# Performance work log

Hardware: AMD Instinct MI355X
Metric: run time of the kernel (lower is better)

## Reference

```python
import jax, jax.numpy as jnp
import numpy as np
from jax.scipy.linalg import solve_triangular

EPS = 2e-05  # module eps (original only adds it on Cholesky failure)
NUM_LABELS = 8


def setup_inputs() -> dict:
    key = jax.random.key(0)
    k1, k2, k3, k4 = jax.random.split(key, 4)
    B, N, H, W = 1, 256, 512, 512
    return {
        "content_feat": jax.random.normal(k1, (B, N, H, W), dtype=jnp.float32),
        "style_feat": jax.random.normal(k2, (B, N, H, W), dtype=jnp.float32),
        "content_seg": jax.random.randint(k3, (H, W), 0, NUM_LABELS, dtype=jnp.int32),
        "style_seg": jax.random.randint(k4, (H, W), 0, NUM_LABELS, dtype=jnp.int32),
        "num_labels": NUM_LABELS,
    }


def _cwct(c, s, seg_c, seg_s, num_labels):
    # c, s: (N, M) flattened features; seg_*: (M,) int labels
    N = c.shape[0]
    eye = jnp.eye(N, dtype=c.dtype)
    target = c
    for l in range(num_labels):  # fixed small label count
        mc = (seg_c == l)  # (Mc,) content mask
        ms = (seg_s == l)
        nc = mc.sum().astype(c.dtype)
        ns = ms.sum().astype(c.dtype)
        nc1 = jnp.maximum(nc, 1.0)
        ns1 = jnp.maximum(ns, 1.0)
        # masked mean + centered (zeros outside mask)
        mean_c = (c * mc).sum(-1) / nc1
        xc = (c - mean_c[:, None]) * mc  # (N, M)
        cov_c = (xc @ xc.T) / jnp.maximum(nc1 - 1.0, 1.0)  # (N, N)
        Lc = jnp.linalg.cholesky(cov_c)
        inv_Lc = solve_triangular(Lc, eye, lower=True)
        white = inv_Lc @ xc
        # style stats + coloring
        mean_s = (s * ms).sum(-1) / ns1
        xs = (s - mean_s[:, None]) * ms
        cov_s = (xs @ xs.T) / jnp.maximum(ns1 - 1.0, 1.0)
        Ls = jnp.linalg.cholesky(cov_s)
        colored = Ls @ white + mean_s[:, None]
        # label validity: >10 pixels each side, count ratio < 100
        valid = (nc > 10) & (ns > 10) & (nc < 100.0 * ns) & (ns < 100.0 * nc)
        target = jnp.where(mc[None, :] & valid, colored, target)
    return target


def reference(content_feat, style_feat, content_seg, style_seg, num_labels):
    B, N, cH, cW = content_feat.shape  # B == 1 (original code only supports B=1)
    c = content_feat.reshape(N, cH * cW)
    s = style_feat.reshape(N, -1)
    out = _cwct(c, s, content_seg.reshape(-1), style_seg.reshape(-1), num_labels)
    return out.reshape(B, N, cH, cW)
```

## Files before the change

### kernel.cpp

```cpp
#include <hip/hip_runtime.h>

#define NCH   256
#define M_PIX 262144
#define MPAD  266240
#define LDA   40

typedef short bf16x8 __attribute__((ext_vector_type(8)));
typedef float f32x4  __attribute__((ext_vector_type(4)));

__device__ __forceinline__ unsigned short f2bf(float f) {
  union { float f; unsigned u; } v; v.f = f;
  unsigned r = v.u + 0x7FFFu + ((v.u >> 16) & 1u);
  return (unsigned short)(r >> 16);
}
__device__ __forceinline__ float bf2f(unsigned short h) {
  union { unsigned u; float f; } v; v.u = ((unsigned)h) << 16;
  return v.f;
}

__global__ __launch_bounds__(256) void k_hist(const int* __restrict__ seg_c,
                                              const int* __restrict__ seg_s,
                                              int* __restrict__ hist) {
  __shared__ int h[16];
  int t = threadIdx.x;
  if (t < 16) h[t] = 0;
  __syncthreads();
  int p0 = blockIdx.x * 2048 + t * 8;
#pragma unroll
  for (int e = 0; e < 8; ++e) {
    atomicAdd(&h[seg_c[p0 + e] & 7], 1);
    atomicAdd(&h[8 + (seg_s[p0 + e] & 7)], 1);
  }
  __syncthreads();
  if (t < 8) hist[blockIdx.x * 8 + t] = h[t];
  else if (t < 16) hist[1024 + blockIdx.x * 8 + (t - 8)] = h[t];
}

__global__ __launch_bounds__(256) void k_scan(const int* __restrict__ hist,
                                              int* __restrict__ base,
                                              int* __restrict__ off,
                                              int* __restrict__ cnt,
                                              int* __restrict__ valid) {
  __shared__ int lh[2048];
  __shared__ int tot[16];
  __shared__ int loff[2][9];
  int t = threadIdx.x;
  for (int i = t; i < 2048; i += 256) lh[i] = hist[i];
  __syncthreads();
  if (t < 16) {
    int s = t >> 3, l = t & 7, acc = 0;
    for (int b = 0; b < 128; ++b) acc += lh[s * 1024 + b * 8 + l];
    tot[t] = acc;
  }
  __syncthreads();
  if (t < 2) {
    int run = 0;
    for (int l = 0; l < 8; ++l) {
      loff[t][l] = run;
      run = (run + tot[t * 8 + l] + 511) & ~511;
    }
    loff[t][8] = run;
    for (int l = 0; l < 9; ++l) off[t * 9 + l] = loff[t][l];
    for (int l = 0; l < 8; ++l) cnt[t * 8 + l] = tot[t * 8 + l];
  }
  __syncthreads();
  if (t < 8) {
    long nc = tot[t], ns = tot[8 + t];
    valid[t] = (nc > 10 && ns > 10 && nc < 100 * ns && ns < 100 * nc) ? 1 : 0;
  }
  if (t < 16) {
    int s = t >> 3, l = t & 7;
    int run = loff[s][l];
    for (int b = 0; b < 128; ++b) {
      base[s * 1024 + b * 8 + l] = run;
      run += lh[s * 1024 + b * 8 + l];
    }
  }
}

__global__ __launch_bounds__(256) void k_rank(const int* __restrict__ seg_c,
                                              const int* __restrict__ seg_s,
                                              const int* __restrict__ base,
                                              int* __restrict__ dst) {
  __shared__ int sc[8 * 272];
  __shared__ int rb[256 * 8];
  __shared__ int bb[8];
  int t = threadIdx.x;
  for (int s = 0; s < 2; ++s) {
    const int* seg = s ? seg_s : seg_c;
    const int* bas = base + s * 1024 + blockIdx.x * 8;
    int* dd = dst + (size_t)s * M_PIX;
    int p0 = blockIdx.x * 2048 + t * 8;
    unsigned pk2 = 0, cpk = 0;
#pragma unroll
    for (int e = 0; e < 8; ++e) {
      int lb = seg[p0 + e] & 7;
      pk2 |= (unsigned)lb << (3 * e);
      cpk += 1u << (4 * lb);
    }
#pragma unroll
    for (int lq = 0; lq < 8; ++lq) sc[lq * 272 + t] = (int)((cpk >> (4 * lq)) & 15u);
    if (t < 8) bb[t] = bas[t];
    __syncthreads();
    for (int d = 1; d < 256; d <<= 1) {
      int v[8];
#pragma unroll
      for (int lq = 0; lq < 8; ++lq)
        v[lq] = sc[lq * 272 + t] + ((t >= d) ? sc[lq * 272 + t - d] : 0);
      __syncthreads();
#pragma unroll
      for (int lq = 0; lq < 8; ++lq) sc[lq * 272 + t] = v[lq];
      __syncthreads();
    }
#pragma unroll
    for (int lq = 0; lq < 8; ++lq)
      rb[t * 8 + lq] = bb[lq] + sc[lq * 272 + t] - (int)((cpk >> (4 * lq)) & 15u);
#pragma unroll
    for (int e = 0; e < 8; ++e) {
      int lb = (int)((pk2 >> (3 * e)) & 7u);
      int dpos = rb[t * 8 + lb]++;
      dd[p0 + e] = dpos;
    }
    __syncthreads();
  }
}

__global__ __launch_bounds__(256) void k_padzero(unsigned short* __restrict__ P,
                                                 const int* __restrict__ off,
                                                 const int* __restrict__ cnt) {
  int l = blockIdx.x;
  int c0, c1;
  if (l < 8) { c0 = off[l] + cnt[l]; c1 = off[l + 1]; }
  else       { c0 = off[8];          c1 = MPAD; }
  int w = c1 - c0;
  if (w <= 0) return;
  for (int r = 0; r < 256; ++r)
    for (int cc = threadIdx.x; cc < w; cc += 256)
      P[(size_t)r * MPAD + c0 + cc] = 0;
}

__global__ __launch_bounds__(256) void k_pack(const float* __restrict__ feat,
                                              const int* __restrict__ seg,
                                              const int* __restrict__ dst,
                                              const int* __restrict__ base,
                                              unsigned short* __restrict__ P) {
  int b = blockIdx.x, g = blockIdx.y, t = threadIdx.x;
  int p0 = b * 2048;
  __shared__ unsigned short buf[8][2048];
  __shared__ int h[8], lbase[9], gbase[8];
  if (t < 8) { h[t] = 0; gbase[t] = base[b * 8 + t]; }
  __syncthreads();
  int lb[8], slot[8], gd[8];
#pragma unroll
  for (int i = 0; i < 8; ++i) {
    lb[i] = seg[p0 + i * 256 + t] & 7;
    atomicAdd(&h[lb[i]], 1);
  }
  __syncthreads();
  if (t == 0) {
    int run = 0;
    for (int l = 0; l < 8; ++l) { lbase[l] = run; run += h[l]; }
    lbase[8] = run;
  }
  __syncthreads();
#pragma unroll
  for (int i = 0; i < 8; ++i)
    slot[i] = lbase[lb[i]] + (dst[p0 + i * 256 + t] - gbase[lb[i]]);
#pragma unroll
  for (int i = 0; i < 8; ++i) {
    int q = i * 256 + t;
    int l = 0;
    while (l < 7 && q >= lbase[l + 1]) ++l;
    gd[i] = gbase[l] + q - lbase[l];
  }
  int n0 = g * 32;
#pragma unroll 1
  for (int cp = 0; cp < 4; ++cp) {
#pragma unroll
    for (int c = 0; c < 8; ++c) {
      const float* fp = &feat[(size_t)(n0 + cp * 8 + c) * M_PIX + p0];
#pragma unroll
      for (int i = 0; i < 8; ++i)
        buf[c][slot[i]] = f2bf(fp[i * 256 + t]);
    }
    __syncthreads();
#pragma unroll
    for (int c = 0; c < 8; ++c) {
      unsigned short* pp = &P[(size_t)(n0 + cp * 8 + c) * MPAD];
#pragma unroll
      for (int i = 0; i < 8; ++i)
        pp[gd[i]] = buf[c][i * 256 + t];
    }
    __syncthreads();
  }
}

__global__ __launch_bounds__(256) void k_unpack(const unsigned short* __restrict__ P,
                                                const int* __restrict__ seg,
                                                const int* __restrict__ dst,
                                                const int* __restrict__ base,
                                                float* __restrict__ out) {
  int b = blockIdx.x, g = blockIdx.y, t = threadIdx.x;
  int p0 = b * 2048;
  __shared__ unsigned short buf[8][2048];
  __shared__ int h[8], lbase[9], gbase[8];
  if (t < 8) { h[t] = 0; gbase[t] = base[b * 8 + t]; }
  __syncthreads();
  int lb[8], slot[8], gd[8];
#pragma unroll
  for (int i = 0; i < 8; ++i) {
    lb[i] = seg[p0 + i * 256 + t] & 7;
    atomicAdd(&h[lb[i]], 1);
  }
  __syncthreads();
  if (t == 0) {
    int run = 0;
    for (int l = 0; l < 8; ++l) { lbase[l] = run; run += h[l]; }
    lbase[8] = run;
  }
  __syncthreads();
#pragma unroll
  for (int i = 0; i < 8; ++i)
    slot[i] = lbase[lb[i]] + (dst[p0 + i * 256 + t] - gbase[lb[i]]);
#pragma unroll
  for (int i = 0; i < 8; ++i) {
    int q = i * 256 + t;
    int l = 0;
    while (l < 7 && q >= lbase[l + 1]) ++l;
    gd[i] = gbase[l] + q - lbase[l];
  }
  int n0 = g * 32;
#pragma unroll 1
  for (int cp = 0; cp < 4; ++cp) {
#pragma unroll
    for (int c = 0; c < 8; ++c) {
      const unsigned short* pp = &P[(size_t)(n0 + cp * 8 + c) * MPAD];
#pragma unroll
      for (int i = 0; i < 8; ++i)
        buf[c][i * 256 + t] = pp[gd[i]];
    }
    __syncthreads();
#pragma unroll
    for (int c = 0; c < 8; ++c) {
      float* op = &out[(size_t)(n0 + cp * 8 + c) * M_PIX + p0];
#pragma unroll
      for (int i = 0; i < 8; ++i)
        op[i * 256 + t] = bf2f(buf[c][slot[i]]);
    }
    __syncthreads();
  }
}

__global__ __launch_bounds__(512) void k_gram(const unsigned short* __restrict__ P,
                                              const int* __restrict__ off,
                                              float* __restrict__ G,
                                              float* __restrict__ sum) {
  int l = blockIdx.y;
  long o0 = off[l], o1 = off[l + 1];
  long k0 = o0 + (long)blockIdx.x * 1024;
  if (k0 >= o1) return;
  long rem = o1 - k0;
  int ks = rem > 1024 ? 1024 : (int)rem;

  __shared__ unsigned short Sb[256 * LDA];
  int t = threadIdx.x, wave = t >> 6, lane = t & 63;
  int wr = (wave < 2) ? wave * 64 : 128 + (wave & 1) * 64;
  int wc = (wave >= 4) ? 128 : 0;
  bool wact = (wave < 6);

  f32x4 acc[4][8] = {};
  float rsum = 0.0f;

  for (int kk = 0; kk < ks; kk += 32) {
#pragma unroll
    for (int it = 0; it < 2; ++it) {
      int slot = t + it * 512;
      int rr = slot >> 2, gg = slot & 3;
      *(uint4*)&Sb[rr * LDA + gg * 8] =
          *(const uint4*)&P[(size_t)rr * MPAD + (size_t)(k0 + kk) + gg * 8];
    }
    __syncthreads();
    if (t < 256) {
#pragma unroll
      for (int e = 0; e < 16; ++e) {
        unsigned v = *(const unsigned*)&Sb[t * LDA + e * 2];
        rsum += bf2f((unsigned short)(v & 0xFFFFu)) + bf2f((unsigned short)(v >> 16));
      }
    }
    if (wact) {
      bf16x8 bfr[8];
#pragma unroll
      for (int fj = 0; fj < 8; ++fj)
        bfr[fj] = *(const bf16x8*)&Sb[(wc + fj * 16 + (lane & 15)) * LDA + (lane >> 4) * 8];
#pragma unroll
      for (int fi = 0; fi < 4; ++fi) {
        bf16x8 afr = *(const bf16x8*)&Sb[(wr + fi * 16 + (lane & 15)) * LDA + (lane >> 4) * 8];
#pragma unroll
        for (int fj = 0; fj < 8; ++fj)
          acc[fi][fj] = __builtin_amdgcn_mfma_f32_16x16x32_bf16(afr, bfr[fj], acc[fi][fj], 0, 0, 0);
      }
    }
    __syncthreads();
  }
  float* Gl = G + ((size_t)l << 16);
  if (wact) {
#pragma unroll
    for (int fi = 0; fi < 4; ++fi)
#pragma unroll
      for (int fj = 0; fj < 8; ++fj) {
        int cc = wc + fj * 16 + (lane & 15);
#pragma unroll
        for (int rg = 0; rg < 4; ++rg) {
          int rr2 = wr + fi * 16 + (lane >> 4) * 4 + rg;
          atomicAdd(&Gl[rr2 * 256 + cc], acc[fi][fj][rg]);
        }
      }
  }
  if (t < 256) atomicAdd(&sum[l * 256 + t], rsum);
}

__global__ __launch_bounds__(256) void k_cov(float* __restrict__ G,
                                             const float* __restrict__ sum,
                                             const int* __restrict__ cnt,
                                             float* __restrict__ means) {
  int bid = blockIdx.x;
  float* A = G + ((size_t)bid << 16);
  int t = threadIdx.x;
  __shared__ float mu[256];
  float fc = (float)cnt[bid];
  float m = sum[bid * 256 + t] / fmaxf(fc, 1.0f);
  mu[t] = m;
  means[bid * 256 + t] = m;
  __syncthreads();
  float rdiv = 1.0f / fmaxf(fmaxf(fc, 1.0f) - 1.0f, 1.0f);
  float mt = mu[t];
  for (int i = t; i < 256; ++i) {
    float g = A[i * 256 + t];
    A[t * 256 + i] = (g - fc * mu[i] * mt) * rdiv;
  }
}

__global__ __launch_bounds__(256) void k_panel(float* __restrict__ G,
                                               float* __restrict__ Wg,
                                               int pb) {
  float* LT = G + ((size_t)blockIdx.x << 16);
  int t = threadIdx.x;
  int jbase = pb * 32;
  int H2 = 224 - jbase;
  __shared__ float Wl[32 * 36];

  if (t < 64) {
    int l32 = t & 31;
    float x[32];
#pragma unroll
    for (int k = 0; k < 32; ++k)
      x[k] = (k <= l32) ? LT[(size_t)(jbase + k) * 256 + jbase + l32] : 0.0f;
#pragma unroll
    for (int j = 0; j < 32; ++j) {
      float dj = __shfl(x[j], j, 64);
      float rd = 1.0f / sqrtf(dj);
      float lj = x[j] * rd;
      x[j] = lj;
#pragma unroll
      for (int k = j + 1; k < 32; ++k) {
        float lkj = __shfl(lj, k, 64);
        x[k] -= lj * lkj;
      }
    }
    if (t < 32) {
#pragma unroll
      for (int k = 0; k < 32; ++k)
        if (k <= l32) LT[(size_t)(jbase + k) * 256 + jbase + l32] = x[k];
    }
    float w[32];
#pragma unroll
    for (int k = 0; k < 32; ++k) w[k] = 0.0f;
#pragma unroll
    for (int i2 = 0; i2 < 32; ++i2) {
      float s = (i2 == l32) ? 1.0f : 0.0f;
#pragma unroll
      for (int k = 0; k < 32; ++k)
        if (k < i2) s -= __shfl(x[k], i2, 64) * w[k];
      float Lii = __shfl(x[i2], i2, 64);
      float wv = s / Lii;
      w[i2] = (i2 >= l32) ? wv : 0.0f;
    }
    if (t < 32) {
      float* Wgp = Wg + (((size_t)blockIdx.x * 8 + pb) << 10);
#pragma unroll
      for (int i2 = 0; i2 < 32; ++i2)
        if (i2 >= l32) {
          Wl[i2 * 36 + l32] = w[i2];
          Wgp[i2 * 32 + l32] = w[i2];
        }
    }
  }
  __syncthreads();

  if (t < H2) {
    int r = jbase + 32 + t;
    float a[32];
#pragma unroll
    for (int k = 0; k < 32; ++k) a[k] = LT[(size_t)(jbase + k) * 256 + r];
#pragma unroll
    for (int j = 0; j < 32; ++j) {
      float s = 0.0f;
#pragma unroll
      for (int k = 0; k < 32; ++k)
        if (k <= j) s += a[k] * Wl[j * 36 + k];
      LT[(size_t)(jbase + j) * 256 + r] = s;
    }
  }
}

__global__ __launch_bounds__(256) void k_trail(float* __restrict__ G, int pb) {
  int jbase = pb * 32;
  int H2 = 224 - jbase;
  int nts2 = (H2 + 63) >> 6;
  int y = blockIdx.y;
  if (y >= (nts2 * (nts2 + 1)) >> 1) return;
  int ti = 0;
  while ((((ti + 1) * (ti + 2)) >> 1) <= y) ++ti;
  int tj = y - ((ti * (ti + 1)) >> 1);
  float* LT = G + ((size_t)blockIdx.x << 16);
  int i0 = jbase + 32 + ti * 64;
  int j0 = jbase + 32 + tj * 64;

  __shared__ float Li[32][64];
  __shared__ float Lj[32][64];
  int t = threadIdx.x;
  for (int idx = t; idx < 2048; idx += 256) {
    int k = idx >> 6, r = idx & 63;
    Li[k][r] = (i0 + r < 256) ? LT[(size_t)(jbase + k) * 256 + i0 + r] : 0.0f;
    Lj[k][r] = (j0 + r < 256) ? LT[(size_t)(jbase + k) * 256 + j0 + r] : 0.0f;
  }
  __syncthreads();

  int tx = t & 15, ty = t >> 4;
  float acc[4][4] = {};
#pragma unroll
  for (int k = 0; k < 32; ++k) {
    float4 a = *(const float4*)&Li[k][ty * 4];
    float4 b = *(const float4*)&Lj[k][tx * 4];
    acc[0][0] += a.x * b.x; acc[0][1] += a.x * b.y; acc[0][2] += a.x * b.z; acc[0][3] += a.x * b.w;
    acc[1][0] += a.y * b.x; acc[1][1] += a.y * b.y; acc[1][2] += a.y * b.z; acc[1][3] += a.y * b.w;
    acc[2][0] += a.z * b.x; acc[2][1] += a.z * b.y; acc[2][2] += a.z * b.z; acc[2][3] += a.z * b.w;
    acc[3][0] += a.w * b.x; acc[3][1] += a.w * b.y; acc[3][2] += a.w * b.z; acc[3][3] += a.w * b.w;
  }
#pragma unroll
  for (int jj = 0; jj < 4; ++jj) {
    int j = j0 + tx * 4 + jj;
    if (j >= 256) continue;
    float* col = &LT[(size_t)j * 256 + i0 + ty * 4];
#pragma unroll
    for (int ii = 0; ii < 4; ++ii) {
      int i = i0 + ty * 4 + ii;
      if (i < 256 && i >= j) col[ii] -= acc[ii][jj];
    }
  }
}

#define RQ_INIT(q, rq)                                                          \
  _Pragma("unroll") for (int kl = 0; kl < 32; ++kl) {                           \
    int kg = h * 128 + q * 32 + kl;                                             \
    rq[kl] = (i >= kg) ? Ls[(size_t)kg * 256 + i] : 0.0f;                       \
  }

#define SOLVE_QW(rq)                                                            \
  _Pragma("unroll") for (int jl = 0; jl < 32; ++jl) {                           \
    float s = 0.0f;                                                             \
    _Pragma("unroll") for (int kl = 0; kl < 32; ++kl)                           \
      if (kl >= jl) s += rq[kl] * Wp[kl * 36 + jl];                             \
    Tp[i * 33 + jl] = s;                                                        \
  }

#define P2Q(q, rq)                                                              \
  if ((h * 128 + q * 32 + 32) <= jbase) {                                       \
    _Pragma("unroll") for (int kg = 0; kg < 8; ++kg) {                          \
      _Pragma("unroll") for (int jl = 0; jl < 32; ++jl) {                       \
        const float4 lc =                                                       \
            *(const float4*)&LcRows[jl * 260 + h * 128 + q * 32 + kg * 4];      \
        rq[kg * 4 + 0] -= tv[jl] * lc.x;                                        \
        rq[kg * 4 + 1] -= tv[jl] * lc.y;                                        \
        rq[kg * 4 + 2] -= tv[jl] * lc.z;                                        \
        rq[kg * 4 + 3] -= tv[jl] * lc.w;                                        \
      }                                                                         \
    }                                                                           \
  }

__global__ __launch_bounds__(512) void k_T(const float* __restrict__ G,
                                           const float* __restrict__ Wg,
                                           const float* __restrict__ means,
                                           const int* __restrict__ valid,
                                           unsigned short* __restrict__ Tb,
                                           float* __restrict__ bvec) {
  int l = blockIdx.x;
  int t = threadIdx.x;
  unsigned short* Tbl = Tb + ((size_t)l << 16);
  if (!valid[l]) {
    for (int x = t; x < 65536; x += 512) {
      int rr = x >> 8, cc = x & 255;
      Tbl[x] = f2bf(rr == cc ? 1.0f : 0.0f);
    }
    if (t < 256) bvec[l * 256 + t] = 0.0f;
    return;
  }
  const float* Lc = G + ((size_t)l << 16);
  const float* Ls = G + ((size_t)(8 + l) << 16);

  __shared__ float Tp[256 * 33];
  __shared__ float LcRows[32 * 260];
  __shared__ float Wp[32 * 36];
  __shared__ float muc[256];

  int i = t & 255, h = t >> 8;

  if (t < 256) muc[t] = means[l * 256 + t];

  float r0[32], r1[32], r2[32], r3[32];
  RQ_INIT(0, r0) RQ_INIT(1, r1) RQ_INIT(2, r2) RQ_INIT(3, r3)
  float bacc = 0.0f;

#pragma unroll 1
  for (int jb = 7; jb >= 0; --jb) {
    int jbase = jb * 32;
    __syncthreads();
    for (int idx = t; idx < 32 * 256; idx += 512) {
      int c = idx >> 5, jl = idx & 31;
      int j = jbase + jl;
      LcRows[jl * 260 + c] = (c <= j) ? Lc[(size_t)c * 256 + j] : 0.0f;
    }
    for (int idx = t; idx < 1024; idx += 512)
      Wp[(idx >> 5) * 36 + (idx & 31)] = Wg[(((size_t)l * 8 + jb) << 10) + idx];
    __syncthreads();

    if (h == (jb >> 2)) {
      int q = jb & 3;
      if (q == 0) { SOLVE_QW(r0) }
      else if (q == 1) { SOLVE_QW(r1) }
      else if (q == 2) { SOLVE_QW(r2) }
      else { SOLVE_QW(r3) }
    }
    __syncthreads();

#pragma unroll
    for (int e = 0; e < 16; ++e) {
      int jl = h * 16 + e;
      Tbl[(size_t)i * 256 + jbase + jl] = f2bf(Tp[i * 33 + jl]);
    }
    if (h == 0) {
#pragma unroll
      for (int jl = 0; jl < 32; ++jl) bacc += Tp[i * 33 + jl] * muc[jbase + jl];
    }

    float tv[32];
#pragma unroll
    for (int jl = 0; jl < 32; ++jl) tv[jl] = Tp[i * 33 + jl];
    P2Q(0, r0) P2Q(1, r1) P2Q(2, r2) P2Q(3, r3)
  }

  if (h == 0) bvec[l * 256 + i] = means[(8 + l) * 256 + i] - bacc;
}

__global__ __launch_bounds__(256) void k_outgemm(unsigned short* __restrict__ P,
                                                 const unsigned short* __restrict__ Tb,
                                                 const float* __restrict__ bvec,
                                                 const int* __restrict__ off) {
  long px0 = (long)blockIdx.x * 128;
  if (px0 >= off[8]) return;
  int l = 0;
  while (l < 7 && px0 >= off[l + 1]) ++l;
  const unsigned short* Tl = Tb + ((size_t)l << 16);

  __shared__ unsigned short As[256 * LDA];
  __shared__ unsigned short Bs[128 * LDA];
  __shared__ float bsh[256];

  int t = threadIdx.x, wave = t >> 6, lane = t & 63;
  int wrow = wave * 64;
  bsh[t] = bvec[l * 256 + t];

  f32x4 acc[4][8] = {};

  for (int kk = 0; kk < 256; kk += 32) {
#pragma unroll
    for (int it = 0; it < 4; ++it) {
      int slot = t + it * 256;
      int rr = slot >> 2, gg = slot & 3;
      *(uint4*)&As[rr * LDA + gg * 8] = *(const uint4*)&Tl[rr * 256 + kk + gg * 8];
    }
#pragma unroll
    for (int it = 0; it < 2; ++it) {
      int slot = t + it * 256;
      int pg = slot & 15, kr = slot >> 4;
      uint4 v = *(const uint4*)&P[(size_t)(kk + kr) * MPAD + px0 + pg * 8];
      const unsigned short* vs = (const unsigned short*)&v;
      int krs = kr ^ ((pg & 3) << 3);
#pragma unroll
      for (int e = 0; e < 8; ++e) Bs[(pg * 8 + e) * LDA + krs] = vs[e];
    }
    __syncthreads();
    if (kk < wrow + 64) {
      bf16x8 bfr[8];
#pragma unroll
      for (int fj = 0; fj < 8; ++fj) {
        int px = fj * 16 + (lane & 15);
        int gs = (lane >> 4) ^ ((px >> 3) & 3);
        bfr[fj] = *(const bf16x8*)&Bs[px * LDA + gs * 8];
      }
#pragma unroll
      for (int fi = 0; fi < 4; ++fi) {
        if (wrow + fi * 16 + 15 >= kk) {
          bf16x8 afr = *(const bf16x8*)&As[(wrow + fi * 16 + (lane & 15)) * LDA + (lane >> 4) * 8];
#pragma unroll
          for (int fj = 0; fj < 8; ++fj)
            acc[fi][fj] = __builtin_amdgcn_mfma_f32_16x16x32_bf16(afr, bfr[fj], acc[fi][fj], 0, 0, 0);
        }
      }
    }
    __syncthreads();
  }
#pragma unroll
  for (int fi = 0; fi < 4; ++fi)
#pragma unroll
    for (int fj = 0; fj < 8; ++fj) {
      long p = px0 + fj * 16 + (lane & 15);
#pragma unroll
      for (int rg = 0; rg < 4; ++rg) {
        int rr = wrow + fi * 16 + (lane >> 4) * 4 + rg;
        float v = acc[fi][fj][rg] + bsh[rr];
        P[(size_t)rr * MPAD + p] = f2bf(v);
      }
    }
}

extern "C" void kernel_launch(void* const* d_in, const int* in_sizes, int n_in,
                              void* d_out, int out_size, void* d_ws, size_t ws_size,
                              hipStream_t stream) {
  const float* cfeat = (const float*)d_in[0];
  const float* sfeat = (const float*)d_in[1];
  const int* seg_c   = (const int*)d_in[2];
  const int* seg_s   = (const int*)d_in[3];

  char* ws = (char*)d_ws;
  size_t o = 0;
  auto take = [&](size_t b) { size_t r = o; o += (b + 255) & ~(size_t)255; return r; };

  unsigned short* P  = (unsigned short*)(ws + take((size_t)NCH * MPAD * 2));
  size_t zero_b = o;
  float* G           = (float*)(ws + take((size_t)2 * 8 * 65536 * 4));
  float* sum         = (float*)(ws + take((size_t)2 * 8 * 256 * 4));
  int*   hist        = (int*)(ws + take((size_t)2 * 128 * 8 * 4));
  size_t zero_e = o;
  unsigned short* Tb = (unsigned short*)(ws + take((size_t)8 * 65536 * 2));
  float* Wg          = (float*)(ws + take((size_t)16 * 8 * 1024 * 4));
  int*   dst         = (int*)(ws + take((size_t)2 * M_PIX * 4));
  float* means       = (float*)(ws + take((size_t)2 * 8 * 256 * 4));
  float* bvec        = (float*)(ws + take((size_t)8 * 256 * 4));
  int*   base        = (int*)(ws + take((size_t)2 * 128 * 8 * 4));
  int*   off         = (int*)(ws + take((size_t)2 * 9 * 4));
  int*   cnt         = (int*)(ws + take((size_t)2 * 8 * 4));
  int*   valid       = (int*)(ws + take((size_t)8 * 4));
  (void)ws_size; (void)n_in; (void)in_sizes; (void)out_size;

  hipMemsetAsync(ws + zero_b, 0, zero_e - zero_b, stream);

  k_hist<<<dim3(128), dim3(256), 0, stream>>>(seg_c, seg_s, hist);
  k_scan<<<dim3(1), dim3(256), 0, stream>>>(hist, base, off, cnt, valid);
  k_rank<<<dim3(128), dim3(256), 0, stream>>>(seg_c, seg_s, base, dst);

  for (int s = 1; s >= 0; --s) {
    const float* feat = s ? sfeat : cfeat;
    const int* seg = s ? seg_s : seg_c;
    k_padzero<<<dim3(9), dim3(256), 0, stream>>>(P, off + s * 9, cnt + s * 8);
    k_pack<<<dim3(128, 8), dim3(256), 0, stream>>>(feat, seg, dst + (size_t)s * M_PIX,
                                                   base + s * 1024, P);
    k_gram<<<dim3(260, 8), dim3(512), 0, stream>>>(P, off + s * 9, G + (size_t)s * 8 * 65536,
                                                   sum + (size_t)s * 8 * 256);
  }

  k_cov<<<dim3(16), dim3(256), 0, stream>>>(G, sum, cnt, means);
  for (int pb = 0; pb < 8; ++pb) {
    k_panel<<<dim3(16), dim3(256), 0, stream>>>(G, Wg, pb);
    if (pb < 7) k_trail<<<dim3(16, 10), dim3(256), 0, stream>>>(G, pb);
  }
  k_T<<<dim3(8), dim3(512), 0, stream>>>(G, Wg, means, valid, Tb, bvec);
  k_outgemm<<<dim3(2080), dim3(256), 0, stream>>>(P, Tb, bvec, off);
  k_unpack<<<dim3(128, 8), dim3(256), 0, stream>>>(P, seg_c, dst, base, (float*)d_out);
}
```

Baseline: 1.156 ms.

## Replace serial triangular solve with recursive blocked inverse and parallel GEMM

Measured after the change: 1.735 ms. 1.5x slower.

```diff
diff --git a/kernel.cpp b/kernel.cpp
--- a/kernel.cpp
+++ b/kernel.cpp
@@ -340,14 +340,14 @@
   }
 }
 
-__global__ __launch_bounds__(256) void k_panel(float* __restrict__ G,
-                                               float* __restrict__ Wg,
-                                               int pb) {
+__global__ __launch_bounds__(512) void k_pstep(float* __restrict__ G,
+                                               float* __restrict__ Wg, int pb) {
   float* LT = G + ((size_t)blockIdx.x << 16);
   int t = threadIdx.x;
   int jbase = pb * 32;
   int H2 = 224 - jbase;
   __shared__ float Wl[32 * 36];
+  __shared__ __align__(16) float L21s[32][232];
 
   if (t < 64) {
     int l32 = t & 31;
@@ -409,157 +409,209 @@
       for (int k = 0; k < 32; ++k)
         if (k <= j) s += a[k] * Wl[j * 36 + k];
       LT[(size_t)(jbase + j) * 256 + r] = s;
-    }
-  }
-}
-
-__global__ __launch_bounds__(256) void k_trail(float* __restrict__ G, int pb) {
-  int jbase = pb * 32;
-  int H2 = 224 - jbase;
-  int nts2 = (H2 + 63) >> 6;
-  int y = blockIdx.y;
-  if (y >= (nts2 * (nts2 + 1)) >> 1) return;
-  int ti = 0;
-  while ((((ti + 1) * (ti + 2)) >> 1) <= y) ++ti;
-  int tj = y - ((ti * (ti + 1)) >> 1);
-  float* LT = G + ((size_t)blockIdx.x << 16);
-  int i0 = jbase + 32 + ti * 64;
-  int j0 = jbase + 32 + tj * 64;
-
-  __shared__ float Li[32][64];
-  __shared__ float Lj[32][64];
+      L21s[j][t] = s;
+    }
+  }
+  __syncthreads();
+
+  if (H2 > 0) {
+    int nts = H2 >> 2;
+    int ntiles = (nts * (nts + 1)) >> 1;
+#pragma unroll 1
+    for (int tile = t; tile < ntiles; tile += 512) {
+      int ti = (int)((sqrtf(8.0f * (float)tile + 1.0f) - 1.0f) * 0.5f);
+      while (((ti * (ti + 1)) >> 1) > tile) --ti;
+      while ((((ti + 1) * (ti + 2)) >> 1) <= tile) ++ti;
+      int tj = tile - ((ti * (ti + 1)) >> 1);
+      int i0 = ti * 4, j0 = tj * 4;
+      float acc[4][4] = {};
+#pragma unroll
+      for (int k = 0; k < 32; ++k) {
+        float4 a = *(const float4*)&L21s[k][i0];
+        float4 b = *(const float4*)&L21s[k][j0];
+        acc[0][0] += a.x * b.x; acc[0][1] += a.x * b.y; acc[0][2] += a.x * b.z; acc[0][3] += a.x * b.w;
+        acc[1][0] += a.y * b.x; acc[1][1] += a.y * b.y; acc[1][2] += a.y * b.z; acc[1][3] += a.y * b.w;
+        acc[2][0] += a.z * b.x; acc[2][1] += a.z * b.y; acc[2][2] += a.z * b.z; acc[2][3] += a.z * b.w;
+        acc[3][0] += a.w * b.x; acc[3][1] += a.w * b.y; acc[3][2] += a.w * b.z; acc[3][3] += a.w * b.w;
+      }
+      int gi0 = jbase + 32 + i0, gj0 = jbase + 32 + j0;
+#pragma unroll
+      for (int c = 0; c < 4; ++c) {
+        int jg = gj0 + c;
+        float* col = &LT[(size_t)jg * 256 + gi0];
+#pragma unroll
+        for (int rr = 0; rr < 4; ++rr)
+          if (gi0 + rr >= jg) col[rr] -= acc[rr][c];
+      }
+    }
+  }
+}
+
+__global__ __launch_bounds__(256) void k_vinit(const float* __restrict__ Wg,
+                                               float* __restrict__ Vinv) {
+  int l = blockIdx.x;
+  float* V = Vinv + ((size_t)l << 16);
+  const float* W = Wg + ((size_t)l * 8) * 1024;
   int t = threadIdx.x;
-  for (int idx = t; idx < 2048; idx += 256) {
-    int k = idx >> 6, r = idx & 63;
-    Li[k][r] = (i0 + r < 256) ? LT[(size_t)(jbase + k) * 256 + i0 + r] : 0.0f;
-    Lj[k][r] = (j0 + r < 256) ? LT[(size_t)(jbase + k) * 256 + j0 + r] : 0.0f;
+  for (int pb = 0; pb < 8; ++pb)
+    for (int idx = t; idx < 1024; idx += 256) {
+      int i = idx >> 5, j = idx & 31;
+      V[(size_t)(pb * 32 + i) * 256 + pb * 32 + j] = (i >= j) ? W[pb * 1024 + idx] : 0.0f;
+    }
+}
+
+template <int N>
+__global__ __launch_bounds__(512) void k_vlevel(const float* __restrict__ G,
+                                                float* __restrict__ Vinv) {
+  constexpr int NP = 256 / (2 * N);
+  constexpr int RPT = N / 32;
+  constexpr int CPT = N / 16;
+  int unit = blockIdx.x;
+  int l = unit / NP, pair = unit % NP;
+  const float* LT = G + ((size_t)l << 16);
+  float* V = Vinv + ((size_t)l << 16);
+  int d = pair * 2 * N;
+  int t = threadIdx.x;
+  int cg = t & 15, rg = t >> 4;
+  int r0 = rg * RPT, c0 = cg * CPT;
+
+  __shared__ float Abuf[N][N + 4];
+  __shared__ float Bbuf[N][N + 4];
+
+  for (int idx = t; idx < N * N; idx += 512) {
+    int k = idx / N, r = idx % N;
+    Abuf[r][k] = LT[(size_t)(d + k) * 256 + d + N + r];
+  }
+  for (int idx = t; idx < N * N; idx += 512) {
+    int k = idx / N, c = idx % N;
+    Bbuf[k][c] = V[(size_t)(d + k) * 256 + d + c];
+  }
+  __syncthreads();
+
+  float acc[RPT][CPT];
+#pragma unroll
+  for (int i = 0; i < RPT; ++i)
+#pragma unroll
+    for (int j = 0; j < CPT; ++j) acc[i][j] = 0.0f;
+  for (int k = 0; k < N; ++k) {
+    float av[RPT];
+#pragma unroll
+    for (int i = 0; i < RPT; ++i) av[i] = Abuf[r0 + i][k];
+#pragma unroll
+    for (int j = 0; j < CPT; ++j) {
+      float bv = Bbuf[k][c0 + j];
+#pragma unroll
+      for (int i = 0; i < RPT; ++i) acc[i][j] += av[i] * bv;
+    }
+  }
+  __syncthreads();
+#pragma unroll
+  for (int i = 0; i < RPT; ++i)
+#pragma unroll
+    for (int j = 0; j < CPT; ++j) Abuf[r0 + i][c0 + j] = acc[i][j];
+  for (int idx = t; idx < N * N; idx += 512) {
+    int r = idx / N, k = idx % N;
+    Bbuf[r][k] = V[(size_t)(d + N + r) * 256 + d + N + k];
+  }
+  __syncthreads();
+
+#pragma unroll
+  for (int i = 0; i < RPT; ++i)
+#pragma unroll
+    for (int j = 0; j < CPT; ++j) acc[i][j] = 0.0f;
+  for (int k = 0; k < N; ++k) {
+    float av[RPT];
+#pragma unroll
+    for (int i = 0; i < RPT; ++i) av[i] = Bbuf[r0 + i][k];
+#pragma unroll
+    for (int j = 0; j < CPT; ++j) {
+      float bv = Abuf[k][c0 + j];
+#pragma unroll
+      for (int i = 0; i < RPT; ++i) acc[i][j] += av[i] * bv;
+    }
+  }
+#pragma unroll
+  for (int i = 0; i < RPT; ++i)
+#pragma unroll
+    for (int j = 0; j < CPT; ++j)
+      V[(size_t)(d + N + r0 + i) * 256 + d + c0 + j] = -acc[i][j];
+}
+
+__global__ __launch_bounds__(256) void k_tgemm(const float* __restrict__ G,
+                                               const float* __restrict__ Vinv,
+                                               const float* __restrict__ means,
+                                               const int* __restrict__ valid,
+                                               unsigned short* __restrict__ Tb,
+                                               float* __restrict__ bacc) {
+  int l = blockIdx.y;
+  int ti = blockIdx.x >> 2, tj = blockIdx.x & 3;
+  unsigned short* Tbl = Tb + ((size_t)l << 16);
+  int i0 = ti * 64, j0 = tj * 64;
+  int t = threadIdx.x;
+  if (!valid[l]) {
+    for (int idx = t; idx < 4096; idx += 256) {
+      int i = idx >> 6, j = idx & 63;
+      Tbl[(size_t)(i0 + i) * 256 + j0 + j] = f2bf((i0 + i) == (j0 + j) ? 1.0f : 0.0f);
+    }
+    return;
+  }
+  if (tj > ti) {
+    for (int idx = t; idx < 4096; idx += 256) {
+      int i = idx >> 6, j = idx & 63;
+      Tbl[(size_t)(i0 + i) * 256 + j0 + j] = 0;
+    }
+    return;
+  }
+  const float* LTs = G + ((size_t)(8 + l) << 16);
+  const float* V = Vinv + ((size_t)l << 16);
+
+  __shared__ float As[64][260];
+  __shared__ __align__(16) float Bs[256][68];
+
+  for (int idx = t; idx < 64 * 256; idx += 256) {
+    int k = idx >> 6, i = idx & 63;
+    As[i][k] = (i0 + i >= k) ? LTs[(size_t)k * 256 + i0 + i] : 0.0f;
+  }
+  for (int idx = t; idx < 64 * 256; idx += 256) {
+    int k = idx >> 6, j = idx & 63;
+    Bs[k][j] = V[(size_t)k * 256 + j0 + j];
   }
   __syncthreads();
 
   int tx = t & 15, ty = t >> 4;
   float acc[4][4] = {};
-#pragma unroll
-  for (int k = 0; k < 32; ++k) {
-    float4 a = *(const float4*)&Li[k][ty * 4];
-    float4 b = *(const float4*)&Lj[k][tx * 4];
-    acc[0][0] += a.x * b.x; acc[0][1] += a.x * b.y; acc[0][2] += a.x * b.z; acc[0][3] += a.x * b.w;
-    acc[1][0] += a.y * b.x; acc[1][1] += a.y * b.y; acc[1][2] += a.y * b.z; acc[1][3] += a.y * b.w;
-    acc[2][0] += a.z * b.x; acc[2][1] += a.z * b.y; acc[2][2] += a.z * b.z; acc[2][3] += a.z * b.w;
-    acc[3][0] += a.w * b.x; acc[3][1] += a.w * b.y; acc[3][2] += a.w * b.z; acc[3][3] += a.w * b.w;
-  }
-#pragma unroll
-  for (int jj = 0; jj < 4; ++jj) {
-    int j = j0 + tx * 4 + jj;
-    if (j >= 256) continue;
-    float* col = &LT[(size_t)j * 256 + i0 + ty * 4];
-#pragma unroll
-    for (int ii = 0; ii < 4; ++ii) {
-      int i = i0 + ty * 4 + ii;
-      if (i < 256 && i >= j) col[ii] -= acc[ii][jj];
-    }
-  }
-}
-
-#define RQ_INIT(q, rq)                                                          \
-  _Pragma("unroll") for (int kl = 0; kl < 32; ++kl) {                           \
-    int kg = h * 128 + q * 32 + kl;                                             \
-    rq[kl] = (i >= kg) ? Ls[(size_t)kg * 256 + i] : 0.0f;                       \
-  }
-
-#define SOLVE_QW(rq)                                                            \
-  _Pragma("unroll") for (int jl = 0; jl < 32; ++jl) {                           \
-    float s = 0.0f;                                                             \
-    _Pragma("unroll") for (int kl = 0; kl < 32; ++kl)                           \
-      if (kl >= jl) s += rq[kl] * Wp[kl * 36 + jl];                             \
-    Tp[i * 33 + jl] = s;                                                        \
-  }
-
-#define P2Q(q, rq)                                                              \
-  if ((h * 128 + q * 32 + 32) <= jbase) {                                       \
-    _Pragma("unroll") for (int kg = 0; kg < 8; ++kg) {                          \
-      _Pragma("unroll") for (int jl = 0; jl < 32; ++jl) {                       \
-        const float4 lc =                                                       \
-            *(const float4*)&LcRows[jl * 260 + h * 128 + q * 32 + kg * 4];      \
-        rq[kg * 4 + 0] -= tv[jl] * lc.x;                                        \
-        rq[kg * 4 + 1] -= tv[jl] * lc.y;                                        \
-        rq[kg * 4 + 2] -= tv[jl] * lc.z;                                        \
-        rq[kg * 4 + 3] -= tv[jl] * lc.w;                                        \
-      }                                                                         \
-    }                                                                           \
-  }
-
-__global__ __launch_bounds__(512) void k_T(const float* __restrict__ G,
-                                           const float* __restrict__ Wg,
-                                           const float* __restrict__ means,
-                                           const int* __restrict__ valid,
-                                           unsigned short* __restrict__ Tb,
-                                           float* __restrict__ bvec) {
-  int l = blockIdx.x;
-  int t = threadIdx.x;
-  unsigned short* Tbl = Tb + ((size_t)l << 16);
-  if (!valid[l]) {
-    for (int x = t; x < 65536; x += 512) {
-      int rr = x >> 8, cc = x & 255;
-      Tbl[x] = f2bf(rr == cc ? 1.0f : 0.0f);
-    }
-    if (t < 256) bvec[l * 256 + t] = 0.0f;
-    return;
-  }
-  const float* Lc = G + ((size_t)l << 16);
-  const float* Ls = G + ((size_t)(8 + l) << 16);
-
-  __shared__ float Tp[256 * 33];
-  __shared__ float LcRows[32 * 260];
-  __shared__ float Wp[32 * 36];
-  __shared__ float muc[256];
-
-  int i = t & 255, h = t >> 8;
-
-  if (t < 256) muc[t] = means[l * 256 + t];
-
-  float r0[32], r1[32], r2[32], r3[32];
-  RQ_INIT(0, r0) RQ_INIT(1, r1) RQ_INIT(2, r2) RQ_INIT(3, r3)
-  float bacc = 0.0f;
-
-#pragma unroll 1
-  for (int jb = 7; jb >= 0; --jb) {
-    int jbase = jb * 32;
-    __syncthreads();
-    for (int idx = t; idx < 32 * 256; idx += 512) {
-      int c = idx >> 5, jl = idx & 31;
-      int j = jbase + jl;
-      LcRows[jl * 260 + c] = (c <= j) ? Lc[(size_t)c * 256 + j] : 0.0f;
-    }
-    for (int idx = t; idx < 1024; idx += 512)
-      Wp[(idx >> 5) * 36 + (idx & 31)] = Wg[(((size_t)l * 8 + jb) << 10) + idx];
-    __syncthreads();
-
-    if (h == (jb >> 2)) {
-      int q = jb & 3;
-      if (q == 0) { SOLVE_QW(r0) }
-      else if (q == 1) { SOLVE_QW(r1) }
-      else if (q == 2) { SOLVE_QW(r2) }
-      else { SOLVE_QW(r3) }
-    }
-    __syncthreads();
-
-#pragma unroll
-    for (int e = 0; e < 16; ++e) {
-      int jl = h * 16 + e;
-      Tbl[(size_t)i * 256 + jbase + jl] = f2bf(Tp[i * 33 + jl]);
-    }
-    if (h == 0) {
-#pragma unroll
-      for (int jl = 0; jl < 32; ++jl) bacc += Tp[i * 33 + jl] * muc[jbase + jl];
-    }
-
-    float tv[32];
-#pragma unroll
-    for (int jl = 0; jl < 32; ++jl) tv[jl] = Tp[i * 33 + jl];
-    P2Q(0, r0) P2Q(1, r1) P2Q(2, r2) P2Q(3, r3)
-  }
-
-  if (h == 0) bvec[l * 256 + i] = means[(8 + l) * 256 + i] - bacc;
+  int klo = j0, khi = i0 + 64;
+  for (int k = klo; k < khi; ++k) {
+    float a0 = As[ty * 4 + 0][k], a1 = As[ty * 4 + 1][k];
+    float a2 = As[ty * 4 + 2][k], a3 = As[ty * 4 + 3][k];
+    float4 b = *(const float4*)&Bs[k][tx * 4];
+    acc[0][0] += a0 * b.x; acc[0][1] += a0 * b.y; acc[0][2] += a0 * b.z; acc[0][3] += a0 * b.w;
+    acc[1][0] += a1 * b.x; acc[1][1] += a1 * b.y; acc[1][2] += a1 * b.z; acc[1][3] += a1 * b.w;
+    acc[2][0] += a2 * b.x; acc[2][1] += a2 * b.y; acc[2][2] += a2 * b.z; acc[2][3] += a2 * b.w;
+    acc[3][0] += a3 * b.x; acc[3][1] += a3 * b.y; acc[3][2] += a3 * b.z; acc[3][3] += a3 * b.w;
+  }
+  float mc[4];
+#pragma unroll
+  for (int cc = 0; cc < 4; ++cc) mc[cc] = means[l * 256 + j0 + tx * 4 + cc];
+#pragma unroll
+  for (int rr = 0; rr < 4; ++rr) {
+    int i = i0 + ty * 4 + rr;
+    float partial = 0.0f;
+#pragma unroll
+    for (int cc = 0; cc < 4; ++cc) {
+      Tbl[(size_t)i * 256 + j0 + tx * 4 + cc] = f2bf(acc[rr][cc]);
+      partial += acc[rr][cc] * mc[cc];
+    }
+    atomicAdd(&bacc[l * 256 + i], partial);
+  }
+}
+
+__global__ __launch_bounds__(256) void k_bvec(const float* __restrict__ means,
+                                              const float* __restrict__ bacc,
+                                              const int* __restrict__ valid,
+                                              float* __restrict__ bvec) {
+  int l = blockIdx.x, i = threadIdx.x;
+  bvec[l * 256 + i] = valid[l] ? (means[(8 + l) * 256 + i] - bacc[l * 256 + i]) : 0.0f;
 }
 
 __global__ __launch_bounds__(256) void k_outgemm(unsigned short* __restrict__ P,
@@ -649,7 +701,9 @@
   unsigned short* P  = (unsigned short*)(ws + take((size_t)NCH * MPAD * 2));
   size_t zero_b = o;
   float* G           = (float*)(ws + take((size_t)2 * 8 * 65536 * 4));
+  float* Vinv        = (float*)(ws + take((size_t)8 * 65536 * 4));
   float* sum         = (float*)(ws + take((size_t)2 * 8 * 256 * 4));
+  float* bacc        = (float*)(ws + take((size_t)8 * 256 * 4));
   int*   hist        = (int*)(ws + take((size_t)2 * 128 * 8 * 4));
   size_t zero_e = o;
   unsigned short* Tb = (unsigned short*)(ws + take((size_t)8 * 65536 * 2));
@@ -680,11 +734,14 @@
   }
 
   k_cov<<<dim3(16), dim3(256), 0, stream>>>(G, sum, cnt, means);
-  for (int pb = 0; pb < 8; ++pb) {
-    k_panel<<<dim3(16), dim3(256), 0, stream>>>(G, Wg, pb);
-    if (pb < 7) k_trail<<<dim3(16, 10), dim3(256), 0, stream>>>(G, pb);
-  }
-  k_T<<<dim3(8), dim3(512), 0, stream>>>(G, Wg, means, valid, Tb, bvec);
+  for (int pb = 0; pb < 8; ++pb)
+    k_pstep<<<dim3(16), dim3(512), 0, stream>>>(G, Wg, pb);
+  k_vinit<<<dim3(8), dim3(256), 0, stream>>>(Wg, Vinv);
+  k_vlevel<32><<<dim3(32), dim3(512), 0, stream>>>(G, Vinv);
+  k_vlevel<64><<<dim3(16), dim3(512), 0, stream>>>(G, Vinv);
+  k_vlevel<128><<<dim3(8), dim3(512), 0, stream>>>(G, Vinv);
+  k_tgemm<<<dim3(16, 8), dim3(256), 0, stream>>>(G, Vinv, means, valid, Tb, bacc);
+  k_bvec<<<dim3(8), dim3(256), 0, stream>>>(means, bacc, valid, bvec);
   k_outgemm<<<dim3(2080), dim3(256), 0, stream>>>(P, Tb, bvec, off);
   k_unpack<<<dim3(128, 8), dim3(256), 0, stream>>>(P, seg_c, dst, base, (float*)d_out);
 }
```
